# Optimization experiments

Hardware: AMD Instinct MI355X
Metric: run time of the kernel (lower is better)

## Reference

```python
import jax, jax.numpy as jnp
import numpy as np

N_E, E_DIM, BETA = 8192, 512, 0.25


def setup_inputs() -> dict:
    key = jax.random.key(0)
    k1, k2 = jax.random.split(key)
    z = jax.random.normal(k1, (16, 1024, E_DIM), dtype=jnp.float32)
    # embedding initialized uniform(-1/n_e, 1/n_e)
    emb_w = jax.random.uniform(k2, (N_E, E_DIM), dtype=jnp.float32,
                               minval=-1.0 / N_E, maxval=1.0 / N_E)
    return {"z": z, "emb_w": emb_w}


def reference(z, emb_w):
    B, T, D = z.shape
    zf = z.reshape(-1, D)  # [BT, D]
    # squared-distance matrix: ||z||^2 + ||e||^2 - 2 z e^T  -> [BT, n_e]
    d = (jnp.sum(zf * zf, axis=1, keepdims=True)
         + jnp.sum(emb_w * emb_w, axis=1)
         - 2.0 * jnp.einsum('bd,nd->bn', zf, emb_w))
    idx = jnp.argmin(d, axis=1)  # [BT]
    z_q = emb_w[idx].reshape(z.shape)  # [B, T, D]
    # legacy=False: beta * commit + codebook term
    loss = (BETA * jnp.mean((jax.lax.stop_gradient(z_q) - z) ** 2)
            + jnp.mean((z_q - jax.lax.stop_gradient(z)) ** 2))
    # straight-through: value equals z_q
    z_q_st = z + jax.lax.stop_gradient(z_q - z)
    idx_out = idx.reshape(B, T)
    v = jnp.var(idx_out.astype(jnp.float32))
    return z_q_st, loss, idx_out, v
```

## Files before the change

kernel.cpp:

```cpp
#include <hip/hip_runtime.h>


#define BT   16384
#define DIMS 512
#define NE   8192
#define NS   4
#define BN   256
#define NTPB (NE / NS / BN)

#define LOSS_OFF 8388608
#define IDX_OFF  8388609
#define V_OFF    8404993

#define BEST_OFF  0
#define ENORM_OFF 131072
#define SUMS_OFF  163840
#define CNT_OFF   163864

typedef __attribute__((ext_vector_type(8))) short short8;
typedef __attribute__((ext_vector_type(4))) float floatx4;

#define AS1(p) ((const __attribute__((address_space(1))) void*)(p))
#define AS3(p) ((__attribute__((address_space(3))) void*)(p))

__device__ __forceinline__ unsigned f2bf(float f) {
    unsigned u = __builtin_bit_cast(unsigned, f);
    u += 0x7FFFu + ((u >> 16) & 1u);
    return u >> 16;
}

__global__ __launch_bounds__(256) void prep_kernel(
    const float* __restrict__ z, const float* __restrict__ emb,
    ushort* __restrict__ zh, ushort* __restrict__ ehh,
    float* __restrict__ enorm, unsigned long long* __restrict__ best,
    double* __restrict__ sums, unsigned* __restrict__ counter)
{
    const int lane = threadIdx.x & 63, w = threadIdx.x >> 6;
    const int b = blockIdx.x;
    if (b < NE / 4) {
        const int row = b * 4 + w;
        const float4* p = (const float4*)(emb + (size_t)row * DIMS + lane * 8);
        float4 a = p[0], bb = p[1];
        uint4 h;
        h.x = f2bf(a.x) | (f2bf(a.y) << 16);
        h.y = f2bf(a.z) | (f2bf(a.w) << 16);
        h.z = f2bf(bb.x) | (f2bf(bb.y) << 16);
        h.w = f2bf(bb.z) | (f2bf(bb.w) << 16);
        *(uint4*)(ehh + (size_t)row * DIMS + lane * 8) = h;
        float s = a.x*a.x + a.y*a.y + a.z*a.z + a.w*a.w
                + bb.x*bb.x + bb.y*bb.y + bb.z*bb.z + bb.w*bb.w;
        #pragma unroll
        for (int off = 32; off > 0; off >>= 1) s += __shfl_down(s, off, 64);
        if (lane == 0) enorm[row] = s;
    } else {
        const int row = (b - NE / 4) * 4 + w;
        const float4* p = (const float4*)(z + (size_t)row * DIMS + lane * 8);
        float4 a = p[0], bb = p[1];
        uint4 h;
        h.x = f2bf(a.x) | (f2bf(a.y) << 16);
        h.y = f2bf(a.z) | (f2bf(a.w) << 16);
        h.z = f2bf(bb.x) | (f2bf(bb.y) << 16);
        h.w = f2bf(bb.z) | (f2bf(bb.w) << 16);
        *(uint4*)(zh + (size_t)row * DIMS + lane * 8) = h;
    }
    const int gid = b * 256 + threadIdx.x;
    if (gid < BT) best[gid] = 0xFFFFFFFFFFFFFFFFULL;
    if (gid == 0) { sums[0] = 0.0; sums[1] = 0.0; sums[2] = 0.0; *counter = 0u; }
}

__global__ __launch_bounds__(256, 2) void argmin_mfma(
    const ushort* __restrict__ zh, const ushort* __restrict__ eh,
    const float* __restrict__ enorm, unsigned long long* __restrict__ best)
{
    __shared__ __align__(16) ushort lds[24576];
    const int t = threadIdx.x;
    const int w = t >> 6, lane = t & 63;
    const int quad = lane >> 4, l15 = lane & 15;
    const int mt = blockIdx.x & 127, ns = blockIdx.x >> 7;
    const int m0 = mt * 128;
    const int wm = (w & 1) * 64, wn = (w >> 1) * 128;

    const int l8 = lane >> 3, c8 = lane & 7;
    const int glane = l8 * DIMS + (c8 ^ l8) * 8;
    const ushort* zA = zh + (size_t)m0 * DIMS;
    int srcoff[12], ldso[12]; bool fromB[12];
    #pragma unroll
    for (int gi = 0; gi < 12; gi++) {
        const int q = w * 12 + gi;
        if (q < 16) { fromB[gi] = false; srcoff[gi] = q * 8 * DIMS + glane; ldso[gi] = q * 512; }
        else { const int c = q - 16; fromB[gi] = true; srcoff[gi] = c * 8 * DIMS + glane; ldso[gi] = 8192 + c * 512; }
    }

    const int px0 = quad ^ (l15 & 7);
    const int px1 = (4 + quad) ^ (l15 & 7);

    float bs[16];
    int   bn_[16];
    #pragma unroll
    for (int k = 0; k < 16; k++) { bs[k] = 3.4e38f; bn_[k] = 0; }

    for (int nt = 0; nt < NTPB; nt++) {
        const int n0 = (ns * NTPB + nt) * BN;
        const ushort* eB = eh + (size_t)n0 * DIMS;

        floatx4 acc[4][8];
        #pragma unroll
        for (int i = 0; i < 4; i++)
            #pragma unroll
            for (int j = 0; j < 8; j++)
                acc[i][j] = (floatx4){0.f, 0.f, 0.f, 0.f};

        for (int k0 = 0; k0 < DIMS; k0 += 64) {
            __syncthreads();
            #pragma unroll
            for (int gi = 0; gi < 12; gi++) {
                const ushort* g = (fromB[gi] ? eB : zA) + srcoff[gi] + k0;
                __builtin_amdgcn_global_load_lds(AS1(g), AS3(&lds[ldso[gi]]), 16, 0, 0);
            }
            __syncthreads();
            #pragma unroll
            for (int kk = 0; kk < 2; kk++) {
                const int po = (kk ? px1 : px0) * 8;
                short8 a[4], b[8];
                #pragma unroll
                for (int i = 0; i < 4; i++)
                    a[i] = *(const short8*)&lds[(wm + i * 16 + l15) * 64 + po];
                #pragma unroll
                for (int j = 0; j < 8; j++)
                    b[j] = *(const short8*)&lds[8192 + (wn + j * 16 + l15) * 64 + po];
                #pragma unroll
                for (int i = 0; i < 4; i++)
                    #pragma unroll
                    for (int j = 0; j < 8; j++)
                        acc[i][j] = __builtin_amdgcn_mfma_f32_16x16x32_bf16(a[i], b[j], acc[i][j], 0, 0, 0);
            }
        }

        #pragma unroll
        for (int j = 0; j < 8; j++) {
            const int n = n0 + wn + j * 16 + l15;
            const float en = enorm[n];
            #pragma unroll
            for (int i = 0; i < 4; i++)
                #pragma unroll
                for (int r = 0; r < 4; r++) {
                    const int k = i * 4 + r;
                    float s = fmaf(-2.0f, acc[i][j][r], en);
                    if (s < bs[k]) { bs[k] = s; bn_[k] = n; }
                }
        }
    }

    #pragma unroll
    for (int i = 0; i < 4; i++)
        #pragma unroll
        for (int r = 0; r < 4; r++) {
            const int k = i * 4 + r;
            unsigned su = __builtin_bit_cast(unsigned, bs[k]);
            su = (su & 0x80000000u) ? ~su : (su | 0x80000000u);
            unsigned long long key = ((unsigned long long)su << 32) | (unsigned)bn_[k];
            #pragma unroll
            for (int off = 1; off < 16; off <<= 1) {
                unsigned long long o = __shfl_xor(key, off, 64);
                key = (o < key) ? o : key;
            }
            if (l15 == 0) atomicMin(&best[m0 + wm + i * 16 + quad * 4 + r], key);
        }
}

__global__ __launch_bounds__(256) void gather_loss_kernel(
    const float* __restrict__ z, const float* __restrict__ emb,
    const unsigned long long* __restrict__ best,
    float* __restrict__ out, double* __restrict__ sums, unsigned* __restrict__ counter)
{
    __shared__ int sIdx[32];
    __shared__ double red[4];
    const int t = threadIdx.x;
    const int row0 = blockIdx.x * 32;
    double myIdxSum = 0.0, myIdxSq = 0.0;
    if (t < 32) {
        int row = row0 + t;
        int idx = (int)(unsigned)(best[row] & 0xFFFFFFFFULL);
        sIdx[t] = idx;
        out[IDX_OFF + row] = (float)idx;
        myIdxSum = (double)idx;
        myIdxSq = (double)idx * (double)idx;
    }
    __syncthreads();
    double acc = 0.0;
    #pragma unroll 4
    for (int i = 0; i < 16; i++) {
        int e = i * 1024 + t * 4;
        int rl = e >> 9;
        int c = e & 511;
        int idx = sIdx[rl];
        float4 zv = *(const float4*)(z + (size_t)(row0 + rl) * DIMS + c);
        float4 ev = *(const float4*)(emb + (size_t)idx * DIMS + c);
        *(float4*)(out + (size_t)(row0 + rl) * DIMS + c) = ev;
        float dx = zv.x - ev.x, dy = zv.y - ev.y;
        float dz = zv.z - ev.z, dw = zv.w - ev.w;
        acc += (double)(dx * dx + dy * dy) + (double)(dz * dz + dw * dw);
    }
    const int lane = t & 63, wv = t >> 6;
    #pragma unroll
    for (int off = 32; off > 0; off >>= 1) {
        acc      += __shfl_down(acc, off, 64);
        myIdxSum += __shfl_down(myIdxSum, off, 64);
        myIdxSq  += __shfl_down(myIdxSq, off, 64);
    }
    if (lane == 0) red[wv] = acc;
    __syncthreads();
    if (t == 0) {
        double tot = red[0] + red[1] + red[2] + red[3];
        atomicAdd(&sums[0], tot);
        atomicAdd(&sums[1], myIdxSum);
        atomicAdd(&sums[2], myIdxSq);
        __threadfence();
        unsigned old = atomicAdd(counter, 1u);
        if (old == gridDim.x - 1) {
            __threadfence();
            double s0 = atomicAdd(&sums[0], 0.0);
            double s1 = atomicAdd(&sums[1], 0.0);
            double s2 = atomicAdd(&sums[2], 0.0);
            out[LOSS_OFF] = (float)(1.25 * s0 / (double)((size_t)BT * DIMS));
            double m = s1 / (double)BT;
            out[V_OFF] = (float)(s2 / (double)BT - m * m);
        }
    }
}

extern "C" void kernel_launch(void* const* d_in, const int* in_sizes, int n_in,
                              void* d_out, int out_size, void* d_ws, size_t ws_size,
                              hipStream_t stream) {
    const float* z = (const float*)d_in[0];
    const float* emb = (const float*)d_in[1];
    float* out = (float*)d_out;
    char* ws = (char*)d_ws;
    unsigned long long* best = (unsigned long long*)(ws + BEST_OFF);
    float* enorm  = (float*)(ws + ENORM_OFF);
    double* sums  = (double*)(ws + SUMS_OFF);
    unsigned* counter = (unsigned*)(ws + CNT_OFF);

    ushort* zh = (ushort*)out;
    ushort* ehh = zh + (size_t)BT * DIMS;

    hipLaunchKernelGGL(prep_kernel, dim3(NE / 4 + BT / 4), dim3(256), 0, stream,
                       z, emb, zh, ehh, enorm, best, sums, counter);
    hipLaunchKernelGGL(argmin_mfma, dim3(128 * NS), dim3(256), 0, stream,
                       zh, ehh, enorm, best);
    hipLaunchKernelGGL(gather_loss_kernel, dim3(BT / 32), dim3(256), 0, stream,
                       z, emb, best, out, sums, counter);
}
```

Before: 271.1 us.

## Restructure argmin GEMM into double-buffered 256x256 tiles with 8 waves

Rewrites the distance GEMM kernel to use 512-thread blocks computing 256x256 tiles. A and B tiles are double-buffered in LDS and prefetched one to two k-steps ahead with global_load_lds, using explicit waitcnt, barriers and priority hints to overlap loads with MFMA. Embedding norms are staged in LDS, and blocks are remapped so that blocks sharing an n-slice land on the same XCD. This is meant to hide global-memory latency and improve operand reuse, at the cost of larger LDS use, lower occupancy, and fragile hand-tuned synchronization.

Measured after the change: 258.4 us. 4.7% less time.

```diff
diff --git a/kernel.cpp b/kernel.cpp
--- a/kernel.cpp
+++ b/kernel.cpp
@@ -7,6 +7,7 @@
 #define NS   4
 #define BN   256
 #define NTPB (NE / NS / BN)
+#define NSTEPS 64
 
 #define LOSS_OFF 8388608
 #define IDX_OFF  8388609
@@ -68,94 +69,177 @@
     if (gid == 0) { sums[0] = 0.0; sums[1] = 0.0; sums[2] = 0.0; *counter = 0u; }
 }
 
-__global__ __launch_bounds__(256, 2) void argmin_mfma(
+
+#define LOADB(AB_, NJ0)                                                        \
+    _Pragma("unroll")                                                          \
+    for (int j2 = 0; j2 < 2; j2++) {                                           \
+        b[j2][0] = *(const short8*)&lds[16384u + (AB_) + bro + ((NJ0) + j2) * 1024 + pxo0]; \
+        b[j2][1] = *(const short8*)&lds[16384u + (AB_) + bro + ((NJ0) + j2) * 1024 + pxo1]; \
+    }
+
+#define PHASE_MID(NJ0)                                                         \
+    __builtin_amdgcn_sched_barrier(0);                                         \
+    __builtin_amdgcn_s_barrier();                                              \
+    asm volatile("s_waitcnt lgkmcnt(0)" ::: "memory");                         \
+    __builtin_amdgcn_sched_barrier(0);                                         \
+    __builtin_amdgcn_s_setprio(1);                                             \
+    _Pragma("unroll")                                                          \
+    for (int kk = 0; kk < 2; kk++)                                             \
+        _Pragma("unroll")                                                      \
+        for (int j2 = 0; j2 < 2; j2++)                                         \
+            _Pragma("unroll")                                                  \
+            for (int mi = 0; mi < 4; mi++)                                     \
+                acc[mi][(NJ0) + j2] = __builtin_amdgcn_mfma_f32_16x16x32_bf16( \
+                    a[mi][kk], b[j2][kk], acc[mi][(NJ0) + j2], 0, 0, 0);       \
+    __builtin_amdgcn_s_setprio(0);
+
+#define STAGE_A(SA_, H_) do {                                                  \
+    const int sa_ = (SA_);                                                     \
+    if (sa_ < NSTEPS) {                                                        \
+        const int k0_ = (sa_ & 7) * 64;                                        \
+        const unsigned al_ = (unsigned)(sa_ & 1) * 32768u                      \
+                           + (unsigned)((((H_) * 128) + w * 8) * 64);          \
+        const ushort* g_ = zA + (size_t)((H_) * 128) * DIMS + soff + k0_;      \
+        __builtin_amdgcn_global_load_lds(AS1(g_), AS3(&lds[al_]), 16, 0, 0);   \
+        __builtin_amdgcn_global_load_lds(AS1(g_ + (size_t)64 * DIMS),          \
+                                         AS3(&lds[al_ + 64 * 64]), 16, 0, 0);  \
+    }                                                                          \
+} while (0)
+
+#define STAGE_B(SB_, H_) do {                                                  \
+    const int sb_ = (SB_);                                                     \
+    if (sb_ < NSTEPS) {                                                        \
+        const int k0_ = (sb_ & 7) * 64;                                        \
+        const unsigned bl_ = 16384u + (unsigned)(sb_ & 1) * 32768u             \
+                           + (unsigned)((((H_) * 128) + w * 8) * 64);          \
+        const ushort* g_ = eh + (size_t)(nsN + (sb_ >> 3) * 256 + (H_) * 128) * DIMS \
+                         + soff + k0_;                                         \
+        __builtin_amdgcn_global_load_lds(AS1(g_), AS3(&lds[bl_]), 16, 0, 0);   \
+        __builtin_amdgcn_global_load_lds(AS1(g_ + (size_t)64 * DIMS),          \
+                                         AS3(&lds[bl_ + 64 * 64]), 16, 0, 0);  \
+    }                                                                          \
+} while (0)
+
+#define STEP(S_, AB_, TM_) do {                                                \
+    const int s_ = (S_);                                                       \
+    short8 a[4][2], b[2][2];                                                   \
+         \
+    _Pragma("unroll")                                                          \
+    for (int mi = 0; mi < 4; mi++) {                                           \
+        a[mi][0] = *(const short8*)&lds[(AB_) + aro + mi * 1024 + pxo0];       \
+        a[mi][1] = *(const short8*)&lds[(AB_) + aro + mi * 1024 + pxo1];       \
+    }                                                                          \
+    LOADB(AB_, 0)                                                              \
+    STAGE_B(s_ + 1, 0);                                                        \
+    PHASE_MID(0)                                                               \
+    __builtin_amdgcn_s_barrier();                                              \
+                                   \
+    LOADB(AB_, 2)                                                              \
+    STAGE_B(s_ + 1, 1);                                                        \
+    PHASE_MID(2)                                                               \
+    __builtin_amdgcn_s_barrier();                                              \
+      \
+    LOADB(AB_, 4)                                                              \
+    STAGE_A(s_ + 2, 0);                                                        \
+    PHASE_MID(4)                                                               \
+    __builtin_amdgcn_s_barrier();                                              \
+            \
+    LOADB(AB_, 6)                                                              \
+    STAGE_A(s_ + 2, 1);                                                        \
+    PHASE_MID(6)                                                               \
+    if ((TM_) == 0) asm volatile("s_waitcnt vmcnt(4)" ::: "memory");           \
+    else if ((TM_) == 1) asm volatile("s_waitcnt vmcnt(0)" ::: "memory");      \
+    __builtin_amdgcn_s_barrier();                                              \
+} while (0)
+
+__global__ __launch_bounds__(512, 2) void argmin_mfma(
     const ushort* __restrict__ zh, const ushort* __restrict__ eh,
     const float* __restrict__ enorm, unsigned long long* __restrict__ best)
 {
-    __shared__ __align__(16) ushort lds[24576];
+    __shared__ __align__(16) ushort lds[69632];
+    float* elds = (float*)&lds[65536];
+
     const int t = threadIdx.x;
     const int w = t >> 6, lane = t & 63;
     const int quad = lane >> 4, l15 = lane & 15;
-    const int mt = blockIdx.x & 127, ns = blockIdx.x >> 7;
-    const int m0 = mt * 128;
-    const int wm = (w & 1) * 64, wn = (w >> 1) * 128;
+
+    const int d = blockIdx.x;
+    const int xcd = d & 7, slot = d >> 3;
+    const int ns = xcd >> 1;
+    const int mt = slot * 2 + (xcd & 1);
+    const int m0 = mt * 256;
+    const int nsN = ns * (NTPB * BN);
+
+    const int wrow = (w & 3) * 64;
+    const int wcol = (w >> 2) * 128;
+
+    {
+        float4 v = *(const float4*)(enorm + nsN + t * 4);
+        *(float4*)(elds + t * 4) = v;
+    }
+    __syncthreads();
 
     const int l8 = lane >> 3, c8 = lane & 7;
-    const int glane = l8 * DIMS + (c8 ^ l8) * 8;
+    const int chunk = c8 ^ l8;
+    const int soff = (w * 8 + l8) * DIMS + chunk * 8;
     const ushort* zA = zh + (size_t)m0 * DIMS;
-    int srcoff[12], ldso[12]; bool fromB[12];
+
+    const int pxo0 = (quad ^ (l15 & 7)) * 8;
+    const int pxo1 = ((4 + quad) ^ (l15 & 7)) * 8;
+    const int aro = (wrow + l15) * 64;
+    const int bro = (wcol + l15) * 64;
+
+    floatx4 acc[4][8];
     #pragma unroll
-    for (int gi = 0; gi < 12; gi++) {
-        const int q = w * 12 + gi;
-        if (q < 16) { fromB[gi] = false; srcoff[gi] = q * 8 * DIMS + glane; ldso[gi] = q * 512; }
-        else { const int c = q - 16; fromB[gi] = true; srcoff[gi] = c * 8 * DIMS + glane; ldso[gi] = 8192 + c * 512; }
-    }
-
-    const int px0 = quad ^ (l15 & 7);
-    const int px1 = (4 + quad) ^ (l15 & 7);
+    for (int mi = 0; mi < 4; mi++)
+        #pragma unroll
+        for (int nj = 0; nj < 8; nj++)
+            acc[mi][nj] = (floatx4){0.f, 0.f, 0.f, 0.f};
 
     float bs[16];
     int   bn_[16];
     #pragma unroll
     for (int k = 0; k < 16; k++) { bs[k] = 3.4e38f; bn_[k] = 0; }
 
-    for (int nt = 0; nt < NTPB; nt++) {
-        const int n0 = (ns * NTPB + nt) * BN;
-        const ushort* eB = eh + (size_t)n0 * DIMS;
-
-        floatx4 acc[4][8];
-        #pragma unroll
-        for (int i = 0; i < 4; i++)
+    STAGE_A(0, 0); STAGE_A(0, 1);
+    STAGE_B(0, 0); STAGE_B(0, 1);
+    STAGE_A(1, 0); STAGE_A(1, 1);
+    asm volatile("s_waitcnt vmcnt(4)" ::: "memory");
+    __builtin_amdgcn_s_barrier();
+
+    for (int sp = 0; sp < NSTEPS; sp += 2) {
+        const int tm1 = (sp != NSTEPS - 2) ? 0 : 1;
+        const int tm2 = (sp != NSTEPS - 2) ? 0 : 2;
+        STEP(sp, 0u, tm1);
+        STEP(sp + 1, 32768u, tm2);
+
+        if ((sp & 7) == 6) {
+            const int nt = sp >> 3;
+            const int ebase = nt * 256 + wcol + l15;
+            const int nbase = nsN + nt * 256 + wcol + l15;
             #pragma unroll
-            for (int j = 0; j < 8; j++)
-                acc[i][j] = (floatx4){0.f, 0.f, 0.f, 0.f};
-
-        for (int k0 = 0; k0 < DIMS; k0 += 64) {
-            __syncthreads();
-            #pragma unroll
-            for (int gi = 0; gi < 12; gi++) {
-                const ushort* g = (fromB[gi] ? eB : zA) + srcoff[gi] + k0;
-                __builtin_amdgcn_global_load_lds(AS1(g), AS3(&lds[ldso[gi]]), 16, 0, 0);
-            }
-            __syncthreads();
-            #pragma unroll
-            for (int kk = 0; kk < 2; kk++) {
-                const int po = (kk ? px1 : px0) * 8;
-                short8 a[4], b[8];
+            for (int nj = 0; nj < 8; nj++) {
+                const float en = elds[ebase + nj * 16];
+                const int n = nbase + nj * 16;
                 #pragma unroll
-                for (int i = 0; i < 4; i++)
-                    a[i] = *(const short8*)&lds[(wm + i * 16 + l15) * 64 + po];
-                #pragma unroll
-                for (int j = 0; j < 8; j++)
-                    b[j] = *(const short8*)&lds[8192 + (wn + j * 16 + l15) * 64 + po];
-                #pragma unroll
-                for (int i = 0; i < 4; i++)
+                for (int mi = 0; mi < 4; mi++) {
                     #pragma unroll
-                    for (int j = 0; j < 8; j++)
-                        acc[i][j] = __builtin_amdgcn_mfma_f32_16x16x32_bf16(a[i], b[j], acc[i][j], 0, 0, 0);
+                    for (int r = 0; r < 4; r++) {
+                        const int k = mi * 4 + r;
+                        const float sc = fmaf(-2.0f, acc[mi][nj][r], en);
+                        if (sc < bs[k]) { bs[k] = sc; bn_[k] = n; }
+                    }
+                    acc[mi][nj] = (floatx4){0.f, 0.f, 0.f, 0.f};
+                }
             }
         }
-
-        #pragma unroll
-        for (int j = 0; j < 8; j++) {
-            const int n = n0 + wn + j * 16 + l15;
-            const float en = enorm[n];
-            #pragma unroll
-            for (int i = 0; i < 4; i++)
-                #pragma unroll
-                for (int r = 0; r < 4; r++) {
-                    const int k = i * 4 + r;
-                    float s = fmaf(-2.0f, acc[i][j][r], en);
-                    if (s < bs[k]) { bs[k] = s; bn_[k] = n; }
-                }
-        }
     }
 
     #pragma unroll
-    for (int i = 0; i < 4; i++)
+    for (int mi = 0; mi < 4; mi++)
         #pragma unroll
         for (int r = 0; r < 4; r++) {
-            const int k = i * 4 + r;
+            const int k = mi * 4 + r;
             unsigned su = __builtin_bit_cast(unsigned, bs[k]);
             su = (su & 0x80000000u) ? ~su : (su | 0x80000000u);
             unsigned long long key = ((unsigned long long)su << 32) | (unsigned)bn_[k];
@@ -164,7 +248,7 @@
                 unsigned long long o = __shfl_xor(key, off, 64);
                 key = (o < key) ? o : key;
             }
-            if (l15 == 0) atomicMin(&best[m0 + wm + i * 16 + quad * 4 + r], key);
+            if (l15 == 0) atomicMin(&best[m0 + wrow + mi * 16 + quad * 4 + r], key);
         }
 }
 
@@ -246,7 +330,7 @@
 
     hipLaunchKernelGGL(prep_kernel, dim3(NE / 4 + BT / 4), dim3(256), 0, stream,
                        z, emb, zh, ehh, enorm, best, sums, counter);
-    hipLaunchKernelGGL(argmin_mfma, dim3(128 * NS), dim3(256), 0, stream,
+    hipLaunchKernelGGL(argmin_mfma, dim3(256), dim3(512), 0, stream,
                        zh, ehh, enorm, best);
     hipLaunchKernelGGL(gather_loss_kernel, dim3(BT / 32), dim3(256), 0, stream,
                        z, emb, best, out, sums, counter);
```
